# Kernel optimization log

Hardware: AMD Instinct MI355X
Metric: run time of the kernel (lower is better)

## Reference

```python
import jax, jax.numpy as jnp
import numpy as np

B, S, V, E, D, C = 128, 256, 50000, 300, 200, 3

def setup_inputs() -> dict:
    key = jax.random.key(0)
    ks = jax.random.split(key, 16)
    std = 0.01  # truncated_normal(stddev=0.01) in the original
    d = {
        'x1': jax.random.randint(ks[0], (B, S), 0, V, dtype=jnp.int32),
        'x2': jax.random.randint(ks[1], (B, S), 0, V, dtype=jnp.int32),
        'len1': jax.random.randint(ks[2], (B,), 1, S + 1, dtype=jnp.int32),
        'len2': jax.random.randint(ks[3], (B,), 1, S + 1, dtype=jnp.int32),
        'emb': jax.random.normal(ks[4], (V, E), jnp.float32),
        'W_proj': jax.random.normal(ks[5], (E, D), jnp.float32) * std,
        'F_W1': jax.random.normal(ks[6], (D, D), jnp.float32) * std,
        'F_b1': jnp.zeros((D,), jnp.float32),
        'F_W2': jax.random.normal(ks[7], (D, D), jnp.float32) * std,
        'F_b2': jnp.zeros((D,), jnp.float32),
        'G_W1': jax.random.normal(ks[8], (2 * D, D), jnp.float32) * std,
        'G_b1': jnp.zeros((D,), jnp.float32),
        'G_W2': jax.random.normal(ks[9], (D, D), jnp.float32) * std,
        'G_b2': jnp.zeros((D,), jnp.float32),
        'H_W1': jax.random.normal(ks[10], (2 * D, D), jnp.float32) * std,
        'H_b1': jnp.zeros((D,), jnp.float32),
        'H_W2': jax.random.normal(ks[11], (D, D), jnp.float32) * std,
        'H_b2': jnp.zeros((D,), jnp.float32),
        'W_out': jax.random.normal(ks[12], (D, C), jnp.float32) * std,
        'b_out': jnp.zeros((C,), jnp.float32),
    }
    return d


def _mlp(x, W1, b1, W2, b2):
    # two dense layers, relu after each (activation_fn defaults to relu)
    h = jax.nn.relu(x @ W1 + b1)
    return jax.nn.relu(h @ W2 + b2)


def reference(x1, x2, len1, len2, emb, W_proj,
              F_W1, F_b1, F_W2, F_b2,
              G_W1, G_b1, G_W2, G_b2,
              H_W1, H_b1, H_W2, H_b2,
              W_out, b_out):
    seq = x1.shape[1]
    # masks: [B, S, 1]
    pos = jnp.arange(seq)
    mask1 = (pos[None, :] < len1[:, None]).astype(jnp.float32)[..., None]
    mask2 = (pos[None, :] < len2[:, None]).astype(jnp.float32)[..., None]

    # embed (L2-normalized table) + project to D
    emb_n = emb * jax.lax.rsqrt(jnp.sum(emb * emb, axis=1, keepdims=True))
    e1, e2 = emb_n[x1], emb_n[x2]          # [B,S,E]
    x1p, x2p = e1 @ W_proj, e2 @ W_proj    # [B,S,D]

    # attend: F(x1) . F(x2) -> [B,S1,S2] (broadcast-mul-reduce == contraction)
    f1 = _mlp(x1p, F_W1, F_b1, F_W2, F_b2)
    f2 = _mlp(x2p, F_W1, F_b1, F_W2, F_b2)
    sim = jnp.einsum('bid,bjd->bij', f1, f2)
    sim = sim * (mask1 * jnp.swapaxes(mask2, 1, 2))  # multiplicative mask (as in source)

    alpha = jnp.einsum('bji,bid->bjd', jax.nn.softmax(jnp.swapaxes(sim, 1, 2), axis=-1), x1p)  # [B,S2,D]
    beta = jnp.einsum('bij,bjd->bid', jax.nn.softmax(sim, axis=-1), x2p)                        # [B,S1,D]

    # compare
    v1 = _mlp(jnp.concatenate([x1p, beta], axis=2), G_W1, G_b1, G_W2, G_b2)
    v2 = _mlp(jnp.concatenate([x2p, alpha], axis=2), G_W1, G_b1, G_W2, G_b2)

    # aggregate
    v1 = jnp.sum(v1 * mask1, axis=1)  # [B,D]
    v2 = jnp.sum(v2 * mask2, axis=1)
    h = _mlp(jnp.concatenate([v1, v2], axis=1), H_W1, H_b1, H_W2, H_b2)
    y_hat = h @ W_out + b_out  # [B,C] logits
    return y_hat
```

## Files before the change

kernel.cpp:

```cpp
#include <hip/hip_runtime.h>
#include <math.h>

#define B_ 128
#define S_ 256
#define V_ 50000
#define E_ 300
#define D_ 200
#define C_ 3
#define P_ 256
#define TOK_ (B_*S_)

typedef __attribute__((ext_vector_type(8))) short bf16x8;
typedef __attribute__((ext_vector_type(4))) float f32x4;

static __device__ __forceinline__ short f2bf(float f) {
  unsigned u = __builtin_bit_cast(unsigned, f);
  u += 0x7fffu + ((u >> 16) & 1u);
  return (short)(u >> 16);
}

__global__ __launch_bounds__(256) void prep_all(
    const float* __restrict__ Wproj, const float* __restrict__ FW1,
    const float* __restrict__ FW2, const float* __restrict__ GW1,
    const float* __restrict__ GW2, const float* __restrict__ HW1,
    const float* __restrict__ HW2,
    const float* __restrict__ Fb1, const float* __restrict__ Fb2,
    const float* __restrict__ Gb1, const float* __restrict__ Gb2,
    const float* __restrict__ Hb1, const float* __restrict__ Hb2,
    const int* __restrict__ x1, const int* __restrict__ x2,
    const int* __restrict__ len1, const int* __restrict__ len2,
    unsigned short* __restrict__ WpT, unsigned short* __restrict__ FW1T,
    unsigned short* __restrict__ FW2T, unsigned short* __restrict__ GW1T,
    unsigned short* __restrict__ GW2T, float* __restrict__ HW1p,
    float* __restrict__ HW2p, float* __restrict__ biases,
    float* __restrict__ v12, int* __restrict__ ids12, int* __restrict__ lens12)
{
  const int blk = blockIdx.x;
  const int tid = threadIdx.x;
  if (blk < 320) {
    int idx = blk * 256 + tid;
    int n = idx / 320, k = idx - n * 320;
    WpT[idx] = (unsigned short)f2bf((k < E_ && n < D_) ? Wproj[k * D_ + n] : 0.0f);
  } else if (blk < 576) {
    int idx = (blk - 320) * 256 + tid;
    int n = idx >> 8, k = idx & 255;
    FW1T[idx] = (unsigned short)f2bf((k < D_ && n < D_) ? FW1[k * D_ + n] : 0.0f);
  } else if (blk < 832) {
    int idx = (blk - 576) * 256 + tid;
    int n = idx >> 8, k = idx & 255;
    FW2T[idx] = (unsigned short)f2bf((k < D_ && n < D_) ? FW2[k * D_ + n] : 0.0f);
  } else if (blk < 1088) {
    int idx = (blk - 832) * 256 + tid;
    int n = idx >> 8, k = idx & 255;
    GW2T[idx] = (unsigned short)f2bf((k < D_ && n < D_) ? GW2[k * D_ + n] : 0.0f);
  } else if (blk < 1600) {
    int idx = (blk - 1088) * 256 + tid;
    int n = idx >> 9, k = idx & 511;
    int sk = (k < 256) ? ((k < D_) ? k : -1) : (((k - 256) < D_) ? (D_ + k - 256) : -1);
    GW1T[idx] = (unsigned short)f2bf((sk >= 0 && n < D_) ? GW1[sk * D_ + n] : 0.0f);
  } else if (blk < 2112) {
    int idx = (blk - 1600) * 256 + tid;
    int r = idx >> 8, c = idx & 255;
    int sr = (r < D_) ? r : ((r >= 256 && r < 256 + D_) ? (r - 56) : -1);
    HW1p[idx] = (sr >= 0 && c < D_) ? HW1[sr * D_ + c] : 0.0f;
  } else if (blk < 2368) {
    int idx = (blk - 2112) * 256 + tid;
    int r = idx >> 8, c = idx & 255;
    HW2p[idx] = (r < D_ && c < D_) ? HW2[r * D_ + c] : 0.0f;
  } else if (blk < 2374) {
    int j = blk - 2368;
    const float* src = (j == 0) ? Fb1 : (j == 1) ? Fb2 : (j == 2) ? Gb1
                      : (j == 3) ? Gb2 : (j == 4) ? Hb1 : Hb2;
    biases[j * 256 + tid] = (tid < D_) ? src[tid] : 0.0f;
  } else if (blk < 2630) {
    v12[(blk - 2374) * 256 + tid] = 0.0f;
  } else if (blk < 2886) {
    int idx = (blk - 2630) * 256 + tid;
    ids12[idx] = (idx < TOK_) ? x1[idx] : x2[idx - TOK_];
  } else {
    if (tid < B_) lens12[tid] = len1[tid];
    else if (tid < 2 * B_) lens12[tid] = len2[tid - B_];
  }
}

__global__ __launch_bounds__(256) void invnorm_kernel(const int* __restrict__ ids,
    const float* __restrict__ emb, float* __restrict__ invn) {
  int tok = blockIdx.x * 4 + (threadIdx.x >> 6);
  int l = threadIdx.x & 63;
  long base = (long)ids[tok] * E_;
  float ss = 0.0f;
  for (int e = l; e < E_; e += 64) { float v = emb[base + e]; ss += v * v; }
  #pragma unroll
  for (int d = 32; d >= 1; d >>= 1) ss += __shfl_xor(ss, d, 64);
  if (l == 0) invn[tok] = 1.0f / sqrtf(ss);
}

__global__ __launch_bounds__(256) void transpose_bf16(
    const unsigned short* __restrict__ in, unsigned short* __restrict__ outp) {
  __shared__ unsigned short t[64][66];
  const int b = blockIdx.x;
  const int r0 = blockIdx.y * 64, c0 = blockIdx.z * 64;
  const unsigned short* src = in + (long)b * S_ * P_;
  unsigned short* dst = outp + (long)b * P_ * S_;
  const int tx = threadIdx.x & 63, ty = threadIdx.x >> 6;
  #pragma unroll
  for (int i = 0; i < 16; ++i)
    t[ty * 16 + i][tx] = src[(long)(r0 + ty * 16 + i) * P_ + c0 + tx];
  __syncthreads();
  #pragma unroll
  for (int i = 0; i < 16; ++i)
    dst[(long)(c0 + ty * 16 + i) * S_ + r0 + tx] = t[tx][ty * 16 + i];
}

__global__ __launch_bounds__(512) void proj_mfma(
    const int* __restrict__ ids, const float* __restrict__ emb,
    const float* __restrict__ invn, const unsigned short* __restrict__ WT,
    unsigned short* __restrict__ outp, int K)
{
  __shared__ unsigned short As[128 * 32];
  __shared__ unsigned short Bs[256 * 32];
  const int tid = threadIdx.x;
  const int lane = tid & 63;
  const int w = tid >> 6;
  const int wr = w >> 2, wc = w & 3;
  const long t0 = (long)blockIdx.x * 128;
  const int g = lane >> 4, ln = lane & 15;

  f32x4 acc[4][4];
  #pragma unroll
  for (int i = 0; i < 4; ++i)
    #pragma unroll
    for (int j = 0; j < 4; ++j) acc[i][j] = (f32x4){0.f, 0.f, 0.f, 0.f};

  const int arow = tid >> 2, aks = tid & 3;
  for (int k0 = 0; k0 < K; k0 += 32) {
    {
      const long t = t0 + arow;
      const long base = (long)ids[t] * E_;
      const float inv = invn[t];
      const int kb = k0 + aks * 8;
      short tmp[8];
      #pragma unroll
      for (int i = 0; i < 8; ++i) {
        const int k = kb + i;
        tmp[i] = f2bf((k < E_) ? emb[base + k] * inv : 0.0f);
      }
      bf16x8 v;
      #pragma unroll
      for (int i = 0; i < 8; ++i) v[i] = tmp[i];
      const int slot = aks ^ ((arow >> 1) & 3);
      *(bf16x8*)&As[arow * 32 + slot * 8] = v;
    }
    #pragma unroll
    for (int cc = 0; cc < 2; ++cc) {
      const int c = tid + cc * 512;
      const int col = c >> 2, ks = c & 3;
      bf16x8 v = *(const bf16x8*)(WT + (long)col * K + k0 + ks * 8);
      const int slot = ks ^ ((col >> 1) & 3);
      *(bf16x8*)&Bs[col * 32 + slot * 8] = v;
    }
    __syncthreads();
    bf16x8 af[4], bfr[4];
    #pragma unroll
    for (int fr = 0; fr < 4; ++fr) {
      const int row = wr * 64 + fr * 16 + ln;
      af[fr] = *(const bf16x8*)&As[row * 32 + ((g ^ ((row >> 1) & 3)) * 8)];
    }
    #pragma unroll
    for (int fc = 0; fc < 4; ++fc) {
      const int col = wc * 64 + fc * 16 + ln;
      bfr[fc] = *(const bf16x8*)&Bs[col * 32 + ((g ^ ((col >> 1) & 3)) * 8)];
    }
    #pragma unroll
    for (int fr = 0; fr < 4; ++fr)
      #pragma unroll
      for (int fc = 0; fc < 4; ++fc)
        acc[fr][fc] = __builtin_amdgcn_mfma_f32_16x16x32_bf16(af[fr], bfr[fc], acc[fr][fc], 0, 0, 0);
    __syncthreads();
  }
  const int g4 = g * 4;
  #pragma unroll
  for (int fc = 0; fc < 4; ++fc) {
    const int col = wc * 64 + fc * 16 + ln;
    #pragma unroll
    for (int fr = 0; fr < 4; ++fr) {
      const long rbase = t0 + wr * 64 + fr * 16 + g4;
      #pragma unroll
      for (int r = 0; r < 4; ++r)
        outp[(rbase + r) * P_ + col] = (unsigned short)f2bf(acc[fr][fc][r]);
    }
  }
}

template<int MODE1, bool AGG>
__global__ __launch_bounds__(1024) void fused_mlp(
    const unsigned short* __restrict__ A1, const unsigned short* __restrict__ A2,
    const unsigned short* __restrict__ W1T, const float* __restrict__ b1,
    const unsigned short* __restrict__ W2T, const float* __restrict__ b2,
    unsigned short* __restrict__ outp, float* __restrict__ aggOut,
    const int* __restrict__ lens, int K1)
{
  __shared__ unsigned short As[128 * 32];
  __shared__ unsigned short Bs[256 * 32];
  __shared__ unsigned short Hs[128 * 256];
  const int tid = threadIdx.x;
  const int lane = tid & 63;
  const int w = tid >> 6;
  const int wr = w >> 3, wc = w & 7;
  const long t0 = (long)blockIdx.x * 128;
  const int g = lane >> 4, ln = lane & 15;
  const int g4 = g * 4;

  f32x4 acc[4][2];
  #pragma unroll
  for (int i = 0; i < 4; ++i)
    #pragma unroll
    for (int j = 0; j < 2; ++j) acc[i][j] = (f32x4){0.f, 0.f, 0.f, 0.f};

  for (int k0 = 0; k0 < K1; k0 += 32) {
    if (tid < 512) {
      const int arow = tid >> 2, aks = tid & 3;
      bf16x8 v;
      if (MODE1 == 2) {
        const unsigned short* src = (k0 < P_) ? (A1 + (t0 + arow) * P_ + k0)
                                              : (A2 + (t0 + arow) * P_ + (k0 - P_));
        v = *(const bf16x8*)(src + aks * 8);
      } else {
        v = *(const bf16x8*)(A1 + (t0 + arow) * P_ + k0 + aks * 8);
      }
      const int slot = aks ^ ((arow >> 1) & 3);
      *(bf16x8*)&As[arow * 32 + slot * 8] = v;
    }
    {
      const int col = tid >> 2, ks = tid & 3;
      bf16x8 v = *(const bf16x8*)(W1T + (long)col * K1 + k0 + ks * 8);
      const int slot = ks ^ ((col >> 1) & 3);
      *(bf16x8*)&Bs[col * 32 + slot * 8] = v;
    }
    __syncthreads();
    bf16x8 af[4], bfr[2];
    #pragma unroll
    for (int fr = 0; fr < 4; ++fr) {
      const int row = wr * 64 + fr * 16 + ln;
      af[fr] = *(const bf16x8*)&As[row * 32 + ((g ^ ((row >> 1) & 3)) * 8)];
    }
    #pragma unroll
    for (int fc = 0; fc < 2; ++fc) {
      const int col = wc * 32 + fc * 16 + ln;
      bfr[fc] = *(const bf16x8*)&Bs[col * 32 + ((g ^ ((col >> 1) & 3)) * 8)];
    }
    #pragma unroll
    for (int fr = 0; fr < 4; ++fr)
      #pragma unroll
      for (int fc = 0; fc < 2; ++fc)
        acc[fr][fc] = __builtin_amdgcn_mfma_f32_16x16x32_bf16(af[fr], bfr[fc], acc[fr][fc], 0, 0, 0);
    __syncthreads();
  }

  #pragma unroll
  for (int fc = 0; fc < 2; ++fc) {
    const int col = wc * 32 + fc * 16 + ln;
    const float bb = b1[col];
    #pragma unroll
    for (int fr = 0; fr < 4; ++fr) {
      #pragma unroll
      for (int r = 0; r < 4; ++r) {
        const int lr = wr * 64 + fr * 16 + g4 + r;
        const float v = fmaxf(acc[fr][fc][r] + bb, 0.0f);
        Hs[lr * 256 + ((col & ~31) | ((((col >> 3) & 3) ^ ((lr >> 1) & 3)) << 3) | (col & 7))] =
            (unsigned short)f2bf(v);
      }
    }
  }

  f32x4 acc2[4][2];
  #pragma unroll
  for (int i = 0; i < 4; ++i)
    #pragma unroll
    for (int j = 0; j < 2; ++j) acc2[i][j] = (f32x4){0.f, 0.f, 0.f, 0.f};

  for (int k0 = 0; k0 < 256; k0 += 32) {
    {
      const int col = tid >> 2, ks = tid & 3;
      bf16x8 v = *(const bf16x8*)(W2T + (long)col * 256 + k0 + ks * 8);
      const int slot = ks ^ ((col >> 1) & 3);
      *(bf16x8*)&Bs[col * 32 + slot * 8] = v;
    }
    __syncthreads();
    bf16x8 af[4], bfr[2];
    #pragma unroll
    for (int fr = 0; fr < 4; ++fr) {
      const int row = wr * 64 + fr * 16 + ln;
      af[fr] = *(const bf16x8*)&Hs[row * 256 + k0 + ((g ^ ((row >> 1) & 3)) * 8)];
    }
    #pragma unroll
    for (int fc = 0; fc < 2; ++fc) {
      const int col = wc * 32 + fc * 16 + ln;
      bfr[fc] = *(const bf16x8*)&Bs[col * 32 + ((g ^ ((col >> 1) & 3)) * 8)];
    }
    #pragma unroll
    for (int fr = 0; fr < 4; ++fr)
      #pragma unroll
      for (int fc = 0; fc < 2; ++fc)
        acc2[fr][fc] = __builtin_amdgcn_mfma_f32_16x16x32_bf16(af[fr], bfr[fc], acc2[fr][fc], 0, 0, 0);
    __syncthreads();
  }

  if (AGG) {
    const int b = (int)(t0 >> 8);
    const int s0 = (int)(t0 & 255);
    const int len = lens[b];
    #pragma unroll
    for (int fc = 0; fc < 2; ++fc) {
      const int col = wc * 32 + fc * 16 + ln;
      const float bb = b2[col];
      float sum = 0.0f;
      #pragma unroll
      for (int fr = 0; fr < 4; ++fr) {
        const int sbase = s0 + wr * 64 + fr * 16 + g4;
        #pragma unroll
        for (int r = 0; r < 4; ++r) {
          if (sbase + r < len) sum += fmaxf(acc2[fr][fc][r] + bb, 0.0f);
        }
      }
      sum += __shfl_xor(sum, 16, 64);
      sum += __shfl_xor(sum, 32, 64);
      if (g == 0) atomicAdd(&aggOut[(long)b * P_ + col], sum);
    }
  } else {
    #pragma unroll
    for (int fc = 0; fc < 2; ++fc) {
      const int col = wc * 32 + fc * 16 + ln;
      const float bb = b2[col];
      #pragma unroll
      for (int fr = 0; fr < 4; ++fr) {
        const long rbase = t0 + wr * 64 + fr * 16 + g4;
        #pragma unroll
        for (int r = 0; r < 4; ++r)
          outp[(rbase + r) * P_ + col] = (unsigned short)f2bf(fmaxf(acc2[fr][fc][r] + bb, 0.0f));
      }
    }
  }
}

__global__ __launch_bounds__(1024) void attend_fused(
    const unsigned short* __restrict__ f12, const unsigned short* __restrict__ x12T,
    const int* __restrict__ lens12, unsigned short* __restrict__ out12)
{
  __shared__ unsigned short As[128 * 32];
  __shared__ unsigned short Bs[256 * 32];
  __shared__ unsigned short Pt[128 * 256];
  __shared__ float redmax[128][8];
  __shared__ float redsum[128][8];

  const int tid = threadIdx.x;
  const int lane = tid & 63;
  const int w = tid >> 6;
  const int wr = w >> 3, wc = w & 7;
  const int b = blockIdx.y;
  const int z = blockIdx.z;
  const int i0 = blockIdx.x * 128;
  const int g = lane >> 4, ln = lane & 15;
  const int g4 = g * 4;

  const unsigned short* Afeat = f12 + (size_t)z * TOK_ * P_;
  const unsigned short* Bfeat = f12 + (size_t)(1 - z) * TOK_ * P_;
  const unsigned short* XT    = x12T + (size_t)(1 - z) * TOK_ * P_;
  unsigned short* outp        = out12 + (size_t)z * TOK_ * P_;
  const int l1 = lens12[z * B_ + b];
  const int l2 = lens12[(1 - z) * B_ + b];

  const unsigned short* Arows = Afeat + ((long)b * S_ + i0) * P_;
  const unsigned short* Brows = Bfeat + (long)b * S_ * P_;

  f32x4 acc[4][2];
  #pragma unroll
  for (int i = 0; i < 4; ++i)
    #pragma unroll
    for (int j = 0; j < 2; ++j) acc[i][j] = (f32x4){0.f, 0.f, 0.f, 0.f};

  for (int k0 = 0; k0 < P_; k0 += 32) {
    if (tid < 512) {
      const int arow = tid >> 2, aks = tid & 3;
      bf16x8 v = *(const bf16x8*)(Arows + (long)arow * P_ + k0 + aks * 8);
      const int slot = aks ^ ((arow >> 1) & 3);
      *(bf16x8*)&As[arow * 32 + slot * 8] = v;
    }
    {
      const int col = tid >> 2, ks = tid & 3;
      bf16x8 v = *(const bf16x8*)(Brows + (long)col * P_ + k0 + ks * 8);
      const int slot = ks ^ ((col >> 1) & 3);
      *(bf16x8*)&Bs[col * 32 + slot * 8] = v;
    }
    __syncthreads();
    bf16x8 af[4], bfr[2];
    #pragma unroll
    for (int fr = 0; fr < 4; ++fr) {
      const int row = wr * 64 + fr * 16 + ln;
      af[fr] = *(const bf16x8*)&As[row * 32 + ((g ^ ((row >> 1) & 3)) * 8)];
    }
    #pragma unroll
    for (int fc = 0; fc < 2; ++fc) {
      const int col = wc * 32 + fc * 16 + ln;
      bfr[fc] = *(const bf16x8*)&Bs[col * 32 + ((g ^ ((col >> 1) & 3)) * 8)];
    }
    #pragma unroll
    for (int fr = 0; fr < 4; ++fr)
      #pragma unroll
      for (int fc = 0; fc < 2; ++fc)
        acc[fr][fc] = __builtin_amdgcn_mfma_f32_16x16x32_bf16(af[fr], bfr[fc], acc[fr][fc], 0, 0, 0);
    __syncthreads();
  }

  #pragma unroll
  for (int fc = 0; fc < 2; ++fc) {
    const int col = wc * 32 + fc * 16 + ln;
    const float mj = (col < l2) ? 1.0f : 0.0f;
    #pragma unroll
    for (int fr = 0; fr < 4; ++fr) {
      #pragma unroll
      for (int r = 0; r < 4; ++r) {
        const int rowg = i0 + wr * 64 + fr * 16 + g4 + r;
        acc[fr][fc][r] *= (rowg < l1) ? mj : 0.0f;
      }
    }
  }
  #pragma unroll
  for (int fr = 0; fr < 4; ++fr) {
    #pragma unroll
    for (int r = 0; r < 4; ++r) {
      float m = fmaxf(acc[fr][0][r], acc[fr][1][r]);
      m = fmaxf(m, __shfl_xor(m, 1, 64));
      m = fmaxf(m, __shfl_xor(m, 2, 64));
      m = fmaxf(m, __shfl_xor(m, 4, 64));
      m = fmaxf(m, __shfl_xor(m, 8, 64));
      if (ln == 0) redmax[wr * 64 + fr * 16 + g4 + r][wc] = m;
    }
  }
  __syncthreads();
  #pragma unroll
  for (int fr = 0; fr < 4; ++fr) {
    #pragma unroll
    for (int r = 0; r < 4; ++r) {
      const int lr = wr * 64 + fr * 16 + g4 + r;
      const float4 a4 = *(const float4*)&redmax[lr][0];
      const float4 b4 = *(const float4*)&redmax[lr][4];
      const float m = fmaxf(fmaxf(fmaxf(a4.x, a4.y), fmaxf(a4.z, a4.w)),
                            fmaxf(fmaxf(b4.x, b4.y), fmaxf(b4.z, b4.w)));
      float s = 0.0f;
      #pragma unroll
      for (int fc = 0; fc < 2; ++fc) {
        const float e = __expf(acc[fr][fc][r] - m);
        acc[fr][fc][r] = e;
        s += e;
      }
      s += __shfl_xor(s, 1, 64);
      s += __shfl_xor(s, 2, 64);
      s += __shfl_xor(s, 4, 64);
      s += __shfl_xor(s, 8, 64);
      if (ln == 0) redsum[lr][wc] = s;
    }
  }
  __syncthreads();
  #pragma unroll
  for (int fr = 0; fr < 4; ++fr) {
    #pragma unroll
    for (int r = 0; r < 4; ++r) {
      const int lr = wr * 64 + fr * 16 + g4 + r;
      const float4 a4 = *(const float4*)&redsum[lr][0];
      const float4 b4 = *(const float4*)&redsum[lr][4];
      const float inv = 1.0f / (a4.x + a4.y + a4.z + a4.w + b4.x + b4.y + b4.z + b4.w);
      #pragma unroll
      for (int fc = 0; fc < 2; ++fc) {
        const int col = wc * 32 + fc * 16 + ln;
        Pt[lr * 256 + ((col & ~31) | ((((col >> 3) & 3) ^ ((lr >> 1) & 3)) << 3) | (col & 7))] =
            (unsigned short)f2bf(acc[fr][fc][r] * inv);
      }
    }
  }

  f32x4 acc2[4][2];
  #pragma unroll
  for (int i = 0; i < 4; ++i)
    #pragma unroll
    for (int j = 0; j < 2; ++j) acc2[i][j] = (f32x4){0.f, 0.f, 0.f, 0.f};
  const unsigned short* XTb = XT + (long)b * P_ * S_;
  for (int k0 = 0; k0 < S_; k0 += 32) {
    {
      const int col = tid >> 2, ks = tid & 3;
      bf16x8 v = *(const bf16x8*)(XTb + (long)col * S_ + k0 + ks * 8);
      const int slot = ks ^ ((col >> 1) & 3);
      *(bf16x8*)&Bs[col * 32 + slot * 8] = v;
    }
    __syncthreads();
    bf16x8 af[4], bfr[2];
    #pragma unroll
    for (int fr = 0; fr < 4; ++fr) {
      const int row = wr * 64 + fr * 16 + ln;
      af[fr] = *(const bf16x8*)&Pt[row * 256 + k0 + ((g ^ ((row >> 1) & 3)) * 8)];
    }
    #pragma unroll
    for (int fc = 0; fc < 2; ++fc) {
      const int col = wc * 32 + fc * 16 + ln;
      bfr[fc] = *(const bf16x8*)&Bs[col * 32 + ((g ^ ((col >> 1) & 3)) * 8)];
    }
    #pragma unroll
    for (int fr = 0; fr < 4; ++fr)
      #pragma unroll
      for (int fc = 0; fc < 2; ++fc)
        acc2[fr][fc] = __builtin_amdgcn_mfma_f32_16x16x32_bf16(af[fr], bfr[fc], acc2[fr][fc], 0, 0, 0);
    __syncthreads();
  }

  #pragma unroll
  for (int fc = 0; fc < 2; ++fc) {
    const int col = wc * 32 + fc * 16 + ln;
    #pragma unroll
    for (int fr = 0; fr < 4; ++fr) {
      const long rbase = (long)b * S_ + i0 + wr * 64 + fr * 16 + g4;
      #pragma unroll
      for (int r = 0; r < 4; ++r)
        outp[(rbase + r) * P_ + col] = (unsigned short)f2bf(acc2[fr][fc][r]);
    }
  }
}

__global__ __launch_bounds__(256) void head_kernel(
    const float* __restrict__ v1s, const float* __restrict__ v2s,
    const float* __restrict__ HW1p, const float* __restrict__ Hb1p,
    const float* __restrict__ HW2p, const float* __restrict__ Hb2p,
    const float* __restrict__ Wout, const float* __restrict__ bout,
    float* __restrict__ y)
{
  __shared__ float xin[2 * P_];
  __shared__ float h[P_];
  const int b = blockIdx.x;
  const int tid = threadIdx.x;
  xin[tid] = v1s[(long)b * P_ + tid];
  xin[P_ + tid] = v2s[(long)b * P_ + tid];
  __syncthreads();
  float acc = Hb1p[tid];
  for (int e = 0; e < 2 * P_; ++e) acc += xin[e] * HW1p[(long)e * P_ + tid];
  h[tid] = fmaxf(acc, 0.0f);
  __syncthreads();
  float acc2 = Hb2p[tid];
  for (int e = 0; e < P_; ++e) acc2 += h[e] * HW2p[(long)e * P_ + tid];
  const float h2 = fmaxf(acc2, 0.0f);
  __syncthreads();
  xin[tid] = h2;
  __syncthreads();
  if (tid < C_) {
    float a = bout[tid];
    for (int d = 0; d < D_; ++d) a += xin[d] * Wout[d * C_ + tid];
    y[(long)b * C_ + tid] = a;
  }
}

extern "C" void kernel_launch(void* const* d_in, const int* in_sizes, int n_in,
                              void* d_out, int out_size, void* d_ws, size_t ws_size,
                              hipStream_t stream)
{
  const int*   x1    = (const int*)d_in[0];
  const int*   x2    = (const int*)d_in[1];
  const int*   len1  = (const int*)d_in[2];
  const int*   len2  = (const int*)d_in[3];
  const float* emb   = (const float*)d_in[4];
  const float* Wproj = (const float*)d_in[5];
  const float* FW1   = (const float*)d_in[6];
  const float* Fb1   = (const float*)d_in[7];
  const float* FW2   = (const float*)d_in[8];
  const float* Fb2   = (const float*)d_in[9];
  const float* GW1   = (const float*)d_in[10];
  const float* Gb1   = (const float*)d_in[11];
  const float* GW2   = (const float*)d_in[12];
  const float* Gb2   = (const float*)d_in[13];
  const float* HW1   = (const float*)d_in[14];
  const float* Hb1   = (const float*)d_in[15];
  const float* HW2   = (const float*)d_in[16];
  const float* Hb2   = (const float*)d_in[17];
  const float* Wout  = (const float*)d_in[18];
  const float* bout  = (const float*)d_in[19];
  float* out = (float*)d_out;

  float* ws = (float*)d_ws;
  size_t o = 0;
  auto alloc = [&](size_t n) { float* p = ws + o; o += n; return p; };
  float* v12    = alloc((size_t)2 * B_ * P_);
  float* invn12 = alloc((size_t)2 * TOK_);
  float* HW1p   = alloc((size_t)2 * P_ * P_);
  float* HW2p   = alloc((size_t)P_ * P_);
  float* biases = alloc((size_t)6 * 256);
  int* ids12  = (int*)alloc((size_t)2 * TOK_);
  int* lens12 = (int*)alloc(2 * B_);
  unsigned short* us = (unsigned short*)(ws + o);
  size_t uo = 0;
  auto ualloc = [&](size_t n) { unsigned short* p = us + uo; uo += n; return p; };
  unsigned short* x12b  = ualloc((size_t)2 * TOK_ * P_);
  unsigned short* f12b  = ualloc((size_t)2 * TOK_ * P_);
  unsigned short* ba12b = ualloc((size_t)2 * TOK_ * P_);
  unsigned short* x12T  = ualloc((size_t)2 * TOK_ * P_);
  unsigned short* WpT   = ualloc((size_t)P_ * 320);
  unsigned short* FW1T  = ualloc((size_t)P_ * P_);
  unsigned short* FW2T  = ualloc((size_t)P_ * P_);
  unsigned short* GW1T  = ualloc((size_t)P_ * 2 * P_);
  unsigned short* GW2T  = ualloc((size_t)P_ * P_);
  if (o * sizeof(float) + uo * sizeof(unsigned short) > ws_size) return;

  float* Fb1p = biases + 0;
  float* Fb2p = biases + 256;
  float* Gb1p = biases + 512;
  float* Gb2p = biases + 768;
  float* Hb1p = biases + 1024;
  float* Hb2p = biases + 1280;
  float* v1s = v12;
  float* v2s = v12 + (size_t)B_ * P_;

  prep_all<<<2887, 256, 0, stream>>>(
      Wproj, FW1, FW2, GW1, GW2, HW1, HW2,
      Fb1, Fb2, Gb1, Gb2, Hb1, Hb2,
      x1, x2, len1, len2,
      WpT, FW1T, FW2T, GW1T, GW2T, HW1p, HW2p, biases, v12, ids12, lens12);

  invnorm_kernel<<<2 * TOK_ / 4, 256, 0, stream>>>(ids12, emb, invn12);

  proj_mfma<<<2 * TOK_ / 128, 512, 0, stream>>>(ids12, emb, invn12, WpT, x12b, 320);

  {
    dim3 grid(2 * B_, 4, 4);
    transpose_bf16<<<grid, 256, 0, stream>>>(x12b, x12T);
  }

  fused_mlp<0, false><<<2 * TOK_ / 128, 1024, 0, stream>>>(
      x12b, nullptr, FW1T, Fb1p, FW2T, Fb2p, f12b, nullptr, nullptr, P_);

  {
    dim3 grid(S_ / 128, B_, 2);
    attend_fused<<<grid, 1024, 0, stream>>>(f12b, x12T, lens12, ba12b);
  }

  fused_mlp<2, true><<<2 * TOK_ / 128, 1024, 0, stream>>>(
      x12b, ba12b, GW1T, Gb1p, GW2T, Gb2p, nullptr, v12, lens12, 2 * P_);

  head_kernel<<<B_, 256, 0, stream>>>(v1s, v2s, HW1p, Hb1p, HW2p, Hb2p, Wout, bout, out);
}
```

Before: 397.6 us.

## Fuse embedding norm into projection and halve row tiles in MLP/attend kernels

Drops the separate inverse-norm kernel and computes each token's embedding L2 norm inside the projection kernel, stored in shared memory. This removes one launch and the global round trip for the norms, at the cost of reading each embedding row once more inside proj. The fused MLP and attention kernels now use 64-row tiles with 512 threads (8 waves along columns) instead of 128 rows with 1024 threads, so there are more, smaller blocks with less LDS each. That should help occupancy and scheduling, but each block reloads the weight/B tiles for fewer rows.

```diff
diff --git a/kernel.cpp b/kernel.cpp
--- a/kernel.cpp
+++ b/kernel.cpp
@@ -83,18 +83,6 @@
   }
 }
 
-__global__ __launch_bounds__(256) void invnorm_kernel(const int* __restrict__ ids,
-    const float* __restrict__ emb, float* __restrict__ invn) {
-  int tok = blockIdx.x * 4 + (threadIdx.x >> 6);
-  int l = threadIdx.x & 63;
-  long base = (long)ids[tok] * E_;
-  float ss = 0.0f;
-  for (int e = l; e < E_; e += 64) { float v = emb[base + e]; ss += v * v; }
-  #pragma unroll
-  for (int d = 32; d >= 1; d >>= 1) ss += __shfl_xor(ss, d, 64);
-  if (l == 0) invn[tok] = 1.0f / sqrtf(ss);
-}
-
 __global__ __launch_bounds__(256) void transpose_bf16(
     const unsigned short* __restrict__ in, unsigned short* __restrict__ outp) {
   __shared__ unsigned short t[64][66];
@@ -114,11 +102,12 @@
 
 __global__ __launch_bounds__(512) void proj_mfma(
     const int* __restrict__ ids, const float* __restrict__ emb,
-    const float* __restrict__ invn, const unsigned short* __restrict__ WT,
+    const unsigned short* __restrict__ WT,
     unsigned short* __restrict__ outp, int K)
 {
   __shared__ unsigned short As[128 * 32];
   __shared__ unsigned short Bs[256 * 32];
+  __shared__ float invn_s[128];
   const int tid = threadIdx.x;
   const int lane = tid & 63;
   const int w = tid >> 6;
@@ -126,6 +115,17 @@
   const long t0 = (long)blockIdx.x * 128;
   const int g = lane >> 4, ln = lane & 15;
 
+  {
+    const int r = tid >> 2, q = tid & 3;
+    const long base = (long)ids[t0 + r] * E_;
+    float ss = 0.0f;
+    for (int e = q; e < E_; e += 4) { float v = emb[base + e]; ss += v * v; }
+    ss += __shfl_xor(ss, 1, 64);
+    ss += __shfl_xor(ss, 2, 64);
+    if (q == 0) invn_s[r] = 1.0f / sqrtf(ss);
+  }
+  __syncthreads();
+
   f32x4 acc[4][4];
   #pragma unroll
   for (int i = 0; i < 4; ++i)
@@ -135,9 +135,8 @@
   const int arow = tid >> 2, aks = tid & 3;
   for (int k0 = 0; k0 < K; k0 += 32) {
     {
-      const long t = t0 + arow;
-      const long base = (long)ids[t] * E_;
-      const float inv = invn[t];
+      const long base = (long)ids[t0 + arow] * E_;
+      const float inv = invn_s[arow];
       const int kb = k0 + aks * 8;
       short tmp[8];
       #pragma unroll
@@ -193,21 +192,20 @@
 }
 
 template<int MODE1, bool AGG>
-__global__ __launch_bounds__(1024) void fused_mlp(
+__global__ __launch_bounds__(512) void fused_mlp(
     const unsigned short* __restrict__ A1, const unsigned short* __restrict__ A2,
     const unsigned short* __restrict__ W1T, const float* __restrict__ b1,
     const unsigned short* __restrict__ W2T, const float* __restrict__ b2,
     unsigned short* __restrict__ outp, float* __restrict__ aggOut,
     const int* __restrict__ lens, int K1)
 {
-  __shared__ unsigned short As[128 * 32];
+  __shared__ unsigned short As[64 * 32];
   __shared__ unsigned short Bs[256 * 32];
-  __shared__ unsigned short Hs[128 * 256];
+  __shared__ unsigned short Hs[64 * 256];
   const int tid = threadIdx.x;
   const int lane = tid & 63;
   const int w = tid >> 6;
-  const int wr = w >> 3, wc = w & 7;
-  const long t0 = (long)blockIdx.x * 128;
+  const long t0 = (long)blockIdx.x * 64;
   const int g = lane >> 4, ln = lane & 15;
   const int g4 = g * 4;
 
@@ -218,7 +216,7 @@
     for (int j = 0; j < 2; ++j) acc[i][j] = (f32x4){0.f, 0.f, 0.f, 0.f};
 
   for (int k0 = 0; k0 < K1; k0 += 32) {
-    if (tid < 512) {
+    if (tid < 256) {
       const int arow = tid >> 2, aks = tid & 3;
       bf16x8 v;
       if (MODE1 == 2) {
@@ -231,8 +229,10 @@
       const int slot = aks ^ ((arow >> 1) & 3);
       *(bf16x8*)&As[arow * 32 + slot * 8] = v;
     }
-    {
-      const int col = tid >> 2, ks = tid & 3;
+    #pragma unroll
+    for (int cc = 0; cc < 2; ++cc) {
+      const int c = tid + cc * 512;
+      const int col = c >> 2, ks = c & 3;
       bf16x8 v = *(const bf16x8*)(W1T + (long)col * K1 + k0 + ks * 8);
       const int slot = ks ^ ((col >> 1) & 3);
       *(bf16x8*)&Bs[col * 32 + slot * 8] = v;
@@ -241,12 +241,12 @@
     bf16x8 af[4], bfr[2];
     #pragma unroll
     for (int fr = 0; fr < 4; ++fr) {
-      const int row = wr * 64 + fr * 16 + ln;
+      const int row = fr * 16 + ln;
       af[fr] = *(const bf16x8*)&As[row * 32 + ((g ^ ((row >> 1) & 3)) * 8)];
     }
     #pragma unroll
     for (int fc = 0; fc < 2; ++fc) {
-      const int col = wc * 32 + fc * 16 + ln;
+      const int col = w * 32 + fc * 16 + ln;
       bfr[fc] = *(const bf16x8*)&Bs[col * 32 + ((g ^ ((col >> 1) & 3)) * 8)];
     }
     #pragma unroll
@@ -259,13 +259,13 @@
 
   #pragma unroll
   for (int fc = 0; fc < 2; ++fc) {
-    const int col = wc * 32 + fc * 16 + ln;
+    const int col = w * 32 + fc * 16 + ln;
     const float bb = b1[col];
     #pragma unroll
     for (int fr = 0; fr < 4; ++fr) {
       #pragma unroll
       for (int r = 0; r < 4; ++r) {
-        const int lr = wr * 64 + fr * 16 + g4 + r;
+        const int lr = fr * 16 + g4 + r;
         const float v = fmaxf(acc[fr][fc][r] + bb, 0.0f);
         Hs[lr * 256 + ((col & ~31) | ((((col >> 3) & 3) ^ ((lr >> 1) & 3)) << 3) | (col & 7))] =
             (unsigned short)f2bf(v);
@@ -280,8 +280,10 @@
     for (int j = 0; j < 2; ++j) acc2[i][j] = (f32x4){0.f, 0.f, 0.f, 0.f};
 
   for (int k0 = 0; k0 < 256; k0 += 32) {
-    {
-      const int col = tid >> 2, ks = tid & 3;
+    #pragma unroll
+    for (int cc = 0; cc < 2; ++cc) {
+      const int c = tid + cc * 512;
+      const int col = c >> 2, ks = c & 3;
       bf16x8 v = *(const bf16x8*)(W2T + (long)col * 256 + k0 + ks * 8);
       const int slot = ks ^ ((col >> 1) & 3);
       *(bf16x8*)&Bs[col * 32 + slot * 8] = v;
@@ -290,12 +292,12 @@
     bf16x8 af[4], bfr[2];
     #pragma unroll
     for (int fr = 0; fr < 4; ++fr) {
-      const int row = wr * 64 + fr * 16 + ln;
+      const int row = fr * 16 + ln;
       af[fr] = *(const bf16x8*)&Hs[row * 256 + k0 + ((g ^ ((row >> 1) & 3)) * 8)];
     }
     #pragma unroll
     for (int fc = 0; fc < 2; ++fc) {
-      const int col = wc * 32 + fc * 16 + ln;
+      const int col = w * 32 + fc * 16 + ln;
       bfr[fc] = *(const bf16x8*)&Bs[col * 32 + ((g ^ ((col >> 1) & 3)) * 8)];
     }
     #pragma unroll
@@ -312,12 +314,12 @@
     const int len = lens[b];
     #pragma unroll
     for (int fc = 0; fc < 2; ++fc) {
-      const int col = wc * 32 + fc * 16 + ln;
+      const int col = w * 32 + fc * 16 + ln;
       const float bb = b2[col];
       float sum = 0.0f;
       #pragma unroll
       for (int fr = 0; fr < 4; ++fr) {
-        const int sbase = s0 + wr * 64 + fr * 16 + g4;
+        const int sbase = s0 + fr * 16 + g4;
         #pragma unroll
         for (int r = 0; r < 4; ++r) {
           if (sbase + r < len) sum += fmaxf(acc2[fr][fc][r] + bb, 0.0f);
@@ -330,11 +332,11 @@
   } else {
     #pragma unroll
     for (int fc = 0; fc < 2; ++fc) {
-      const int col = wc * 32 + fc * 16 + ln;
+      const int col = w * 32 + fc * 16 + ln;
       const float bb = b2[col];
       #pragma unroll
       for (int fr = 0; fr < 4; ++fr) {
-        const long rbase = t0 + wr * 64 + fr * 16 + g4;
+        const long rbase = t0 + fr * 16 + g4;
         #pragma unroll
         for (int r = 0; r < 4; ++r)
           outp[(rbase + r) * P_ + col] = (unsigned short)f2bf(fmaxf(acc2[fr][fc][r] + bb, 0.0f));
@@ -343,23 +345,22 @@
   }
 }
 
-__global__ __launch_bounds__(1024) void attend_fused(
+__global__ __launch_bounds__(512) void attend_fused(
     const unsigned short* __restrict__ f12, const unsigned short* __restrict__ x12T,
     const int* __restrict__ lens12, unsigned short* __restrict__ out12)
 {
-  __shared__ unsigned short As[128 * 32];
+  __shared__ unsigned short As[64 * 32];
   __shared__ unsigned short Bs[256 * 32];
-  __shared__ unsigned short Pt[128 * 256];
-  __shared__ float redmax[128][8];
-  __shared__ float redsum[128][8];
+  __shared__ unsigned short Pt[64 * 256];
+  __shared__ float redmax[64][8];
+  __shared__ float redsum[64][8];
 
   const int tid = threadIdx.x;
   const int lane = tid & 63;
   const int w = tid >> 6;
-  const int wr = w >> 3, wc = w & 7;
   const int b = blockIdx.y;
   const int z = blockIdx.z;
-  const int i0 = blockIdx.x * 128;
+  const int i0 = blockIdx.x * 64;
   const int g = lane >> 4, ln = lane & 15;
   const int g4 = g * 4;
 
@@ -380,14 +381,16 @@
     for (int j = 0; j < 2; ++j) acc[i][j] = (f32x4){0.f, 0.f, 0.f, 0.f};
 
   for (int k0 = 0; k0 < P_; k0 += 32) {
-    if (tid < 512) {
+    if (tid < 256) {
       const int arow = tid >> 2, aks = tid & 3;
       bf16x8 v = *(const bf16x8*)(Arows + (long)arow * P_ + k0 + aks * 8);
       const int slot = aks ^ ((arow >> 1) & 3);
       *(bf16x8*)&As[arow * 32 + slot * 8] = v;
     }
-    {
-      const int col = tid >> 2, ks = tid & 3;
+    #pragma unroll
+    for (int cc = 0; cc < 2; ++cc) {
+      const int c = tid + cc * 512;
+      const int col = c >> 2, ks = c & 3;
       bf16x8 v = *(const bf16x8*)(Brows + (long)col * P_ + k0 + ks * 8);
       const int slot = ks ^ ((col >> 1) & 3);
       *(bf16x8*)&Bs[col * 32 + slot * 8] = v;
@@ -396,12 +399,12 @@
     bf16x8 af[4], bfr[2];
     #pragma unroll
     for (int fr = 0; fr < 4; ++fr) {
-      const int row = wr * 64 + fr * 16 + ln;
+      const int row = fr * 16 + ln;
       af[fr] = *(const bf16x8*)&As[row * 32 + ((g ^ ((row >> 1) & 3)) * 8)];
     }
     #pragma unroll
     for (int fc = 0; fc < 2; ++fc) {
-      const int col = wc * 32 + fc * 16 + ln;
+      const int col = w * 32 + fc * 16 + ln;
       bfr[fc] = *(const bf16x8*)&Bs[col * 32 + ((g ^ ((col >> 1) & 3)) * 8)];
     }
     #pragma unroll
@@ -414,13 +417,13 @@
 
   #pragma unroll
   for (int fc = 0; fc < 2; ++fc) {
-    const int col = wc * 32 + fc * 16 + ln;
+    const int col = w * 32 + fc * 16 + ln;
     const float mj = (col < l2) ? 1.0f : 0.0f;
     #pragma unroll
     for (int fr = 0; fr < 4; ++fr) {
       #pragma unroll
       for (int r = 0; r < 4; ++r) {
-        const int rowg = i0 + wr * 64 + fr * 16 + g4 + r;
+        const int rowg = i0 + fr * 16 + g4 + r;
         acc[fr][fc][r] *= (rowg < l1) ? mj : 0.0f;
       }
     }
@@ -434,7 +437,7 @@
       m = fmaxf(m, __shfl_xor(m, 2, 64));
       m = fmaxf(m, __shfl_xor(m, 4, 64));
       m = fmaxf(m, __shfl_xor(m, 8, 64));
-      if (ln == 0) redmax[wr * 64 + fr * 16 + g4 + r][wc] = m;
+      if (ln == 0) redmax[fr * 16 + g4 + r][w] = m;
     }
   }
   __syncthreads();
@@ -442,7 +445,7 @@
   for (int fr = 0; fr < 4; ++fr) {
     #pragma unroll
     for (int r = 0; r < 4; ++r) {
-      const int lr = wr * 64 + fr * 16 + g4 + r;
+      const int lr = fr * 16 + g4 + r;
       const float4 a4 = *(const float4*)&redmax[lr][0];
       const float4 b4 = *(const float4*)&redmax[lr][4];
       const float m = fmaxf(fmaxf(fmaxf(a4.x, a4.y), fmaxf(a4.z, a4.w)),
@@ -458,7 +461,7 @@
       s += __shfl_xor(s, 2, 64);
       s += __shfl_xor(s, 4, 64);
       s += __shfl_xor(s, 8, 64);
-      if (ln == 0) redsum[lr][wc] = s;
+      if (ln == 0) redsum[lr][w] = s;
     }
   }
   __syncthreads();
@@ -466,13 +469,13 @@
   for (int fr = 0; fr < 4; ++fr) {
     #pragma unroll
     for (int r = 0; r < 4; ++r) {
-      const int lr = wr * 64 + fr * 16 + g4 + r;
+      const int lr = fr * 16 + g4 + r;
       const float4 a4 = *(const float4*)&redsum[lr][0];
       const float4 b4 = *(const float4*)&redsum[lr][4];
       const float inv = 1.0f / (a4.x + a4.y + a4.z + a4.w + b4.x + b4.y + b4.z + b4.w);
       #pragma unroll
       for (int fc = 0; fc < 2; ++fc) {
-        const int col = wc * 32 + fc * 16 + ln;
+        const int col = w * 32 + fc * 16 + ln;
         Pt[lr * 256 + ((col & ~31) | ((((col >> 3) & 3) ^ ((lr >> 1) & 3)) << 3) | (col & 7))] =
             (unsigned short)f2bf(acc[fr][fc][r] * inv);
       }
@@ -486,8 +489,10 @@
     for (int j = 0; j < 2; ++j) acc2[i][j] = (f32x4){0.f, 0.f, 0.f, 0.f};
   const unsigned short* XTb = XT + (long)b * P_ * S_;
   for (int k0 = 0; k0 < S_; k0 += 32) {
-    {
-      const int col = tid >> 2, ks = tid & 3;
+    #pragma unroll
+    for (int cc = 0; cc < 2; ++cc) {
+      const int c = tid + cc * 512;
+      const int col = c >> 2, ks = c & 3;
       bf16x8 v = *(const bf16x8*)(XTb + (long)col * S_ + k0 + ks * 8);
       const int slot = ks ^ ((col >> 1) & 3);
       *(bf16x8*)&Bs[col * 32 + slot * 8] = v;
@@ -496,12 +501,12 @@
     bf16x8 af[4], bfr[2];
     #pragma unroll
     for (int fr = 0; fr < 4; ++fr) {
-      const int row = wr * 64 + fr * 16 + ln;
+      const int row = fr * 16 + ln;
       af[fr] = *(const bf16x8*)&Pt[row * 256 + k0 + ((g ^ ((row >> 1) & 3)) * 8)];
     }
     #pragma unroll
     for (int fc = 0; fc < 2; ++fc) {
-      const int col = wc * 32 + fc * 16 + ln;
+      const int col = w * 32 + fc * 16 + ln;
       bfr[fc] = *(const bf16x8*)&Bs[col * 32 + ((g ^ ((col >> 1) & 3)) * 8)];
     }
     #pragma unroll
@@ -514,10 +519,10 @@
 
   #pragma unroll
   for (int fc = 0; fc < 2; ++fc) {
-    const int col = wc * 32 + fc * 16 + ln;
-    #pragma unroll
-    for (int fr = 0; fr < 4; ++fr) {
-      const long rbase = (long)b * S_ + i0 + wr * 64 + fr * 16 + g4;
+    const int col = w * 32 + fc * 16 + ln;
+    #pragma unroll
+    for (int fr = 0; fr < 4; ++fr) {
+      const long rbase = (long)b * S_ + i0 + fr * 16 + g4;
       #pragma unroll
       for (int r = 0; r < 4; ++r)
         outp[(rbase + r) * P_ + col] = (unsigned short)f2bf(acc2[fr][fc][r]);
@@ -586,7 +591,6 @@
   size_t o = 0;
   auto alloc = [&](size_t n) { float* p = ws + o; o += n; return p; };
   float* v12    = alloc((size_t)2 * B_ * P_);
-  float* invn12 = alloc((size_t)2 * TOK_);
   float* HW1p   = alloc((size_t)2 * P_ * P_);
   float* HW2p   = alloc((size_t)P_ * P_);
   float* biases = alloc((size_t)6 * 256);
@@ -621,24 +625,22 @@
       x1, x2, len1, len2,
       WpT, FW1T, FW2T, GW1T, GW2T, HW1p, HW2p, biases, v12, ids12, lens12);
 
-  invnorm_kernel<<<2 * TOK_ / 4, 256, 0, stream>>>(ids12, emb, invn12);
-
-  proj_mfma<<<2 * TOK_ / 128, 512, 0, stream>>>(ids12, emb, invn12, WpT, x12b, 320);
+  proj_mfma<<<2 * TOK_ / 128, 512, 0, stream>>>(ids12, emb, WpT, x12b, 320);
 
   {
     dim3 grid(2 * B_, 4, 4);
     transpose_bf16<<<grid, 256, 0, stream>>>(x12b, x12T);
   }
 
-  fused_mlp<0, false><<<2 * TOK_ / 128, 1024, 0, stream>>>(
+  fused_mlp<0, false><<<2 * TOK_ / 64, 512, 0, stream>>>(
       x12b, nullptr, FW1T, Fb1p, FW2T, Fb2p, f12b, nullptr, nullptr, P_);
 
   {
-    dim3 grid(S_ / 128, B_, 2);
-    attend_fused<<<grid, 1024, 0, stream>>>(f12b, x12T, lens12, ba12b);
-  }
-
-  fused_mlp<2, true><<<2 * TOK_ / 128, 1024, 0, stream>>>(
+    dim3 grid(S_ / 64, B_, 2);
+    attend_fused<<<grid, 512, 0, stream>>>(f12b, x12T, lens12, ba12b);
+  }
+
+  fused_mlp<2, true><<<2 * TOK_ / 64, 512, 0, stream>>>(
       x12b, ba12b, GW1T, Gb1p, GW2T, Gb2p, nullptr, v12, lens12, 2 * P_);
 
   head_kernel<<<B_, 256, 0, stream>>>(v1s, v2s, HW1p, Hb1p, HW2p, Hb2p, Wout, bout, out);
```

After: 394.4 us. About the same (-0.8%).
